# Optimization experiments

Measured on AMD Instinct MI355X. Metric: run time of the kernel, lower is better.

## Reference

```python
import jax, jax.numpy as jnp
import numpy as np

DIM = 512
N_HEADS = 8
HEAD_DIM = DIM // N_HEADS
BN_EPS = 1e-5


def setup_inputs() -> dict:
    key = jax.random.key(0)
    ks = jax.random.split(key, 8)
    B, C, H, W = 16, DIM, 32, 32
    x = jax.random.normal(ks[0], (B, C, H, W), dtype=jnp.float32)
    # 1x1 convs == channel matmuls: stacked q/k/v weights [3, out, in], proj [out, in]
    w_qkv = jax.random.normal(ks[1], (3, DIM, DIM), dtype=jnp.float32) * (DIM ** -0.5)
    w_proj = jax.random.normal(ks[2], (DIM, DIM), dtype=jnp.float32) * (DIM ** -0.5)
    # BatchNorm (inference form) params for q/k/v branches, stacked [3, C]
    bn_gamma = jax.random.uniform(ks[3], (3, DIM), minval=0.5, maxval=1.5)
    bn_beta = jax.random.normal(ks[4], (3, DIM)) * 0.1
    bn_mean = jax.random.normal(ks[5], (3, DIM)) * 0.1
    bn_var = jax.random.uniform(ks[6], (3, DIM), minval=0.5, maxval=1.5)
    return {"x": x, "w_qkv": w_qkv, "w_proj": w_proj, "bn_gamma": bn_gamma,
            "bn_beta": bn_beta, "bn_mean": bn_mean, "bn_var": bn_var}


def _ternary_ste(t):
    # forward: sign(t) in {-1,0,1}; backward: identity (straight-through)
    return t + jax.lax.stop_gradient(jnp.sign(t) - t)


def reference(x, w_qkv, w_proj, bn_gamma, bn_beta, bn_mean, bn_var):
    B, C, H, W = x.shape
    N = H * W
    xf = x.reshape(B, C, N)
    # fused 1x1 conv for q,k,v: [3,B,C,N]
    qkv = jnp.einsum('koc,bcn->kbon', w_qkv, xf)
    # BatchNorm (inference): y = (x - mean)/sqrt(var+eps)*gamma + beta
    s = bn_gamma / jnp.sqrt(bn_var + BN_EPS)          # [3,C]
    b = bn_beta - bn_mean * s                          # [3,C]
    qkv = qkv * s[:, None, :, None] + b[:, None, :, None]
    q = _ternary_ste(qkv[0]).reshape(B, N_HEADS, HEAD_DIM, N)
    k = _ternary_ste(qkv[1]).reshape(B, N_HEADS, HEAD_DIM, N)
    v = qkv[2].reshape(B, N_HEADS, HEAD_DIM, N)
    scale = HEAD_DIM ** -0.5
    attn = jnp.einsum('bhdn,bhen->bhde', q, k) * scale  # [B,h,d,d] channel-wise attn
    attn = jax.nn.softmax(attn, axis=-1)
    out = jnp.einsum('bhde,bhen->bhdn', attn, v).reshape(B, C, N)
    out = jnp.einsum('oc,bcn->bon', w_proj, out) + xf   # proj + residual
    return out.reshape(B, C, H, W)
```

## Files before the change

### kernel.cpp

```cpp
#include <hip/hip_runtime.h>
#include <math.h>

#define BN_EPS 1e-5f
#define FIXC 1.0e-4f

typedef _Float16 f16;
typedef _Float16 f16x4 __attribute__((ext_vector_type(4)));
typedef _Float16 f16x8 __attribute__((ext_vector_type(8)));
typedef float f32x4 __attribute__((ext_vector_type(4)));
typedef int i32x4 __attribute__((ext_vector_type(4)));

static constexpr int BB = 16;
static constexpr int C  = 512;
static constexpr int NP = 1024;
static constexpr int NH = 8;
static constexpr int HD = 64;
static constexpr int M3 = 1536;

static constexpr size_t OFF_WHI  = 0;
static constexpr size_t OFF_WLO  = 1572864;
static constexpr size_t OFF_WPH  = 3145728;
static constexpr size_t OFF_SB   = 3670016;
static constexpr size_t OFF_WN   = 3682304;
static constexpr size_t OFF_XN   = 3686400;
static constexpr size_t OFF_FLAG = 3751936;
static constexpr size_t OFF_XTH  = 5849088;
static constexpr size_t OFF_XTL  = 22626304;
static constexpr size_t OFF_AOT  = OFF_XTH;
static constexpr size_t OFF_Q    = 39403520;
static constexpr size_t OFF_K    = 47792128;
static constexpr size_t OFF_VT   = 56180736;

__device__ __forceinline__ void gld16(const void* g, void* l) {
  __builtin_amdgcn_global_load_lds(
      (const __attribute__((address_space(1))) void*)g,
      (__attribute__((address_space(3))) void*)l, 16, 0, 0);
}

__global__ __launch_bounds__(256) void k_convW(
    const float* __restrict__ wqkv, const float* __restrict__ wproj,
    const float* __restrict__ g, const float* __restrict__ be,
    const float* __restrict__ mu, const float* __restrict__ va,
    f16* __restrict__ Whi, f16* __restrict__ Wlo, f16* __restrict__ Wph,
    float* __restrict__ sA, float* __restrict__ bA)
{
  const int i = blockIdx.x * 256 + threadIdx.x;
  if (i < M3 * C) {
    const float w = wqkv[i];
    const f16 h = (f16)w;
    Whi[i] = h;
    Wlo[i] = (f16)(w - (float)h);
  }
  if (i < C * C) Wph[i] = (f16)wproj[i];
  if (i < M3) {
    const float s = g[i] / sqrtf(va[i] + BN_EPS);
    sA[i] = s;
    bA[i] = be[i] - mu[i] * s;
  }
}

__global__ __launch_bounds__(256) void k_wnorm(
    const float* __restrict__ wqkv, float* __restrict__ wnorm)
{
  const int row = blockIdx.x * 4 + (threadIdx.x >> 6);
  const int lane = threadIdx.x & 63;
  const float4 v0 = *(const float4*)&wqkv[(size_t)row * C + lane * 8];
  const float4 v1 = *(const float4*)&wqkv[(size_t)row * C + lane * 8 + 4];
  float s = v0.x * v0.x + v0.y * v0.y + v0.z * v0.z + v0.w * v0.w
          + v1.x * v1.x + v1.y * v1.y + v1.z * v1.z + v1.w * v1.w;
  s += __shfl_xor(s, 1);  s += __shfl_xor(s, 2);  s += __shfl_xor(s, 4);
  s += __shfl_xor(s, 8);  s += __shfl_xor(s, 16); s += __shfl_xor(s, 32);
  if (lane == 0) wnorm[row] = sqrtf(s);
}

__global__ __launch_bounds__(256) void k_convX(
    const float* __restrict__ x, f16* __restrict__ XtH, f16* __restrict__ XtL,
    float* __restrict__ xnorm2)
{
  const int k0 = blockIdx.x * 64, n0 = blockIdx.y * 64, b = blockIdx.z;
  __shared__ float ls[64][65];
  const int t = threadIdx.x;
  const float* xp = x + ((size_t)b * C + k0) * NP + n0;
  const int c4 = (t & 15) * 4, r0 = t >> 4;
#pragma unroll
  for (int q = 0; q < 4; ++q) {
    const float4 v = *(const float4*)(xp + (size_t)(r0 + q * 16) * NP + c4);
    ls[r0 + q * 16][c4 + 0] = v.x; ls[r0 + q * 16][c4 + 1] = v.y;
    ls[r0 + q * 16][c4 + 2] = v.z; ls[r0 + q * 16][c4 + 3] = v.w;
  }
  __syncthreads();
  if (t < 64) {
    float s2 = 0.f;
#pragma unroll
    for (int q = 0; q < 64; ++q) { const float v = ls[q][t]; s2 = fmaf(v, v, s2); }
    atomicAdd(&xnorm2[(b << 10) + n0 + t], s2);
  }
  const int n = t >> 2, kk = (t & 3) * 16;
  f16x8 hv0 = {}, hv1 = {}, lv0 = {}, lv1 = {};
#pragma unroll
  for (int q = 0; q < 8; ++q) {
    float v = ls[kk + q][n];
    f16 h = (f16)v;
    hv0[q] = h; lv0[q] = (f16)(v - (float)h);
  }
#pragma unroll
  for (int q = 0; q < 8; ++q) {
    float v = ls[kk + 8 + q][n];
    f16 h = (f16)v;
    hv1[q] = h; lv1[q] = (f16)(v - (float)h);
  }
  const size_t o = ((size_t)b * NP + n0 + n) * C + k0 + kk;
  *(f16x8*)&XtH[o] = hv0; *(f16x8*)&XtH[o + 8] = hv1;
  *(f16x8*)&XtL[o] = lv0; *(f16x8*)&XtL[o + 8] = lv1;
}

__global__ __launch_bounds__(256) void k_qkv_mfma(
    const f16* __restrict__ Whi, const f16* __restrict__ XtH,
    const float* __restrict__ sA, const float* __restrict__ bA,
    const float* __restrict__ wnorm, const float* __restrict__ xnorm2,
    signed char* __restrict__ qw, signed char* __restrict__ kw,
    f16* __restrict__ vt, unsigned* __restrict__ flagbits)
{
  __shared__ __align__(16) f16 SMEM[16384];
  f16* Ah = SMEM;
  f16* Bh = SMEM + 8192;

  const int t = threadIdx.x, lane = t & 63, wid = t >> 6;
  const int n0 = blockIdx.x * 128, m0 = blockIdx.y * 128, b = blockIdx.z;

  const f16* A0h = Whi + (size_t)m0 * C;
  const f16* B0h = XtH + ((size_t)b * NP + n0) * C;

  f32x4 acc[4][4];
#pragma unroll
  for (int i = 0; i < 4; ++i)
#pragma unroll
    for (int j = 0; j < 4; ++j) acc[i][j] = (f32x4){0.f, 0.f, 0.f, 0.f};

  const int wm = wid >> 1, wn = wid & 1;
  const int lr = lane & 15, ls = lane >> 4;
  const int srow8 = wid * 8 + (lane >> 3);
  const int scol = (lane & 7) * 8;

  for (int kc = 0; kc < 512; kc += 64) {
#pragma unroll
    for (int r = 0; r < 4; ++r) {
      const size_t go = (size_t)(r * 32 + srow8) * C + kc + scol;
      const int lo = (r * 32 + wid * 8) * 64;
      gld16(A0h + go, &Ah[lo]);
      gld16(B0h + go, &Bh[lo]);
    }
    __syncthreads();
#pragma unroll
    for (int ksub = 0; ksub < 2; ++ksub) {
      f16x8 ah[4], bh[4];
#pragma unroll
      for (int i = 0; i < 4; ++i) {
        ah[i] = *(const f16x8*)&Ah[(wm * 64 + i * 16 + lr) * 64 + ksub * 32 + ls * 8];
        bh[i] = *(const f16x8*)&Bh[(wn * 64 + i * 16 + lr) * 64 + ksub * 32 + ls * 8];
      }
#pragma unroll
      for (int i = 0; i < 4; ++i)
#pragma unroll
        for (int j = 0; j < 4; ++j)
          acc[i][j] = __builtin_amdgcn_mfma_f32_16x16x32_f16(ah[i], bh[j], acc[i][j], 0, 0, 0);
    }
    __syncthreads();
  }

  const int kidx = m0 >> 9;
  if (kidx != 2) {
    signed char* dst0 = (kidx == 0) ? qw : kw;
    float xnrm[4];
#pragma unroll
    for (int j = 0; j < 4; ++j)
      xnrm[j] = sqrtf(xnorm2[(b << 10) + n0 + wn * 64 + j * 16 + lr]);
#pragma unroll
    for (int i = 0; i < 4; ++i) {
      float sv[4], bv[4], dl[4];
#pragma unroll
      for (int r = 0; r < 4; ++r) {
        const int o = m0 + wm * 64 + i * 16 + ls * 4 + r;
        sv[r] = sA[o]; bv[r] = bA[o];
        dl[r] = FIXC * wnorm[o] * sv[r];
      }
      const int oc0 = (m0 & 511) + wm * 64 + i * 16 + ls * 4;
      const int og0 = m0 + wm * 64 + i * 16 + ls * 4;
#pragma unroll
      for (int j = 0; j < 4; ++j) {
        const int n = n0 + wn * 64 + j * 16 + lr;
#pragma unroll
        for (int r = 0; r < 4; ++r) {
          const float z = fmaf(acc[i][j][r], sv[r], bv[r]);
          dst0[((size_t)b * C + oc0 + r) * NP + n] =
              (signed char)((z > 0.f) - (z < 0.f));
          if (fabsf(z) <= dl[r] * xnrm[j]) {
            const int of = og0 + r;
            atomicOr(&flagbits[(((size_t)b * NP + n) << 5) + (of >> 5)],
                     1u << (of & 31));
          }
        }
      }
    }
  } else {
    const int c0 = m0 & 511;
    for (int hf = 0; hf < 2; ++hf) {
      __syncthreads();
      if (wn == hf) {
#pragma unroll
        for (int i = 0; i < 4; ++i) {
          float sv[4], bv[4];
#pragma unroll
          for (int r = 0; r < 4; ++r) {
            const int o = m0 + wm * 64 + i * 16 + ls * 4 + r;
            sv[r] = sA[o]; bv[r] = bA[o];
          }
#pragma unroll
          for (int j = 0; j < 4; ++j) {
            f16x4 pk;
#pragma unroll
            for (int r = 0; r < 4; ++r)
              pk[r] = (f16)fmaf(acc[i][j][r], sv[r], bv[r]);
            *(f16x4*)&SMEM[(size_t)(j * 16 + lr) * 136 + wm * 64 + i * 16 + ls * 4] = pk;
          }
        }
      }
      __syncthreads();
      const int nl = t >> 2, cc = (t & 3) * 32;
      const f16* src = &SMEM[(size_t)nl * 136 + cc];
      f16x8 r0 = *(const f16x8*)(src + 0);
      f16x8 r1 = *(const f16x8*)(src + 8);
      f16x8 r2 = *(const f16x8*)(src + 16);
      f16x8 r3 = *(const f16x8*)(src + 24);
      f16* dstv = vt + ((size_t)b * NP + n0 + hf * 64 + nl) * C + c0 + cc;
      *(f16x8*)(dstv + 0)  = r0;
      *(f16x8*)(dstv + 8)  = r1;
      *(f16x8*)(dstv + 16) = r2;
      *(f16x8*)(dstv + 24) = r3;
    }
  }
}

__global__ __launch_bounds__(256) void k_fix(
    const unsigned* __restrict__ flagbits,
    const f16* __restrict__ Whi, const f16* __restrict__ Wlo,
    const f16* __restrict__ XtH, const f16* __restrict__ XtL,
    const float* __restrict__ sA, const float* __restrict__ bA,
    signed char* __restrict__ qw, signed char* __restrict__ kw)
{
  const int wv = blockIdx.x * 4 + (threadIdx.x >> 6);
  const int lane = threadIdx.x & 63;
  const int b = wv >> 10, n = wv & 1023;

  const unsigned* bm = flagbits + ((size_t)wv << 5);
  const unsigned myw = (lane < 32) ? bm[lane] : 0u;
  if (__ballot(myw != 0) == 0ULL) return;

  const size_t xo = ((size_t)b * NP + n) * C + lane * 8;
  const f16x8 bhv = *(const f16x8*)&XtH[xo];
  const f16x8 blv = *(const f16x8*)&XtL[xo];
  float xv[8];
#pragma unroll
  for (int q = 0; q < 8; ++q) xv[q] = (float)bhv[q] + (float)blv[q];

  for (int w = 0; w < 32; ++w) {
    unsigned bits = __shfl(myw, w);
    while (bits) {
      const int o = w * 32 + __builtin_ctz(bits);
      bits &= bits - 1;
      const f16x8 ahv = *(const f16x8*)&Whi[(size_t)o * C + lane * 8];
      const f16x8 alv = *(const f16x8*)&Wlo[(size_t)o * C + lane * 8];
      float s = 0.f;
#pragma unroll
      for (int q = 0; q < 8; ++q)
        s = fmaf((float)ahv[q] + (float)alv[q], xv[q], s);
      s += __shfl_xor(s, 1);  s += __shfl_xor(s, 2);  s += __shfl_xor(s, 4);
      s += __shfl_xor(s, 8);  s += __shfl_xor(s, 16); s += __shfl_xor(s, 32);
      if (lane == 0) {
        const float y = fmaf(s, sA[o], bA[o]);
        const signed char sg = (signed char)((y > 0.f) - (y < 0.f));
        if (o < 512) qw[((size_t)b * C + o) * NP + n] = sg;
        else         kw[((size_t)b * C + (o - 512)) * NP + n] = sg;
      }
    }
  }
}

__global__ __launch_bounds__(256) void k_attn_fused(
    const signed char* __restrict__ qw, const signed char* __restrict__ kw,
    const f16* __restrict__ vt, f16* __restrict__ aot)
{
  const int half = blockIdx.x;
  const int bh = blockIdx.y;
  const int b = bh >> 3, h = bh & 7;
  const int t = threadIdx.x, lane = t & 63, wid = t >> 6;
  const int dw = wid * 16;
  const int lr = lane & 15, lg = lane >> 4;

  __shared__ f16 ph[64][72];
  __shared__ f16 pl[64][72];
  __shared__ f16 sb[64][72];

  const signed char* qp = qw + ((size_t)b * C + h * HD + dw + lr) * NP;
  const signed char* kp = kw + ((size_t)b * C + h * HD + lr) * NP;

  i32x4 accS[4];
#pragma unroll
  for (int j = 0; j < 4; ++j) accS[j] = (i32x4){0, 0, 0, 0};

#pragma unroll 4
  for (int ks = 0; ks < 16; ++ks) {
    const i32x4 af = *(const i32x4*)(qp + ks * 64 + lg * 16);
#pragma unroll
    for (int j = 0; j < 4; ++j) {
      const i32x4 bf = *(const i32x4*)(kp + (size_t)(j * 16) * NP + ks * 64 + lg * 16);
      accS[j] = __builtin_amdgcn_mfma_i32_16x16x64_i8(af, bf, accS[j], 0, 0, 0);
    }
  }

#pragma unroll
  for (int r = 0; r < 4; ++r) {
    float mx = (float)accS[0][r];
#pragma unroll
    for (int j = 1; j < 4; ++j) mx = fmaxf(mx, (float)accS[j][r]);
    mx = fmaxf(mx, __shfl_xor(mx, 1));
    mx = fmaxf(mx, __shfl_xor(mx, 2));
    mx = fmaxf(mx, __shfl_xor(mx, 4));
    mx = fmaxf(mx, __shfl_xor(mx, 8));
    float pvv[4];
    float sm = 0.f;
#pragma unroll
    for (int j = 0; j < 4; ++j) {
      pvv[j] = expf(((float)accS[j][r] - mx) * 0.125f);
      sm += pvv[j];
    }
    sm += __shfl_xor(sm, 1);
    sm += __shfl_xor(sm, 2);
    sm += __shfl_xor(sm, 4);
    sm += __shfl_xor(sm, 8);
    const float inv = 1.f / sm;
    const int drow = dw + lg * 4 + r;
#pragma unroll
    for (int j = 0; j < 4; ++j) {
      const float p = pvv[j] * inv;
      const f16 hi = (f16)p;
      ph[drow][j * 16 + lr] = hi;
      pl[drow][j * 16 + lr] = (f16)(p - (float)hi);
    }
  }
  __syncthreads();

  const f16x8 pa0h = *(const f16x8*)&ph[dw + lr][lg * 8];
  const f16x8 pa0l = *(const f16x8*)&pl[dw + lr][lg * 8];
  const f16x8 pa1h = *(const f16x8*)&ph[dw + lr][32 + lg * 8];
  const f16x8 pa1l = *(const f16x8*)&pl[dw + lr][32 + lg * 8];

  const f16* vbase = vt + (size_t)b * NP * C + h * HD;
  const int nbase = half * 512;

  for (int nc = 0; nc < 8; ++nc) {
    const int nn0 = nbase + nc * 64;
    __syncthreads();
#pragma unroll
    for (int nt = 0; nt < 4; ++nt) {
      const f16* vp = vbase + (size_t)(nn0 + nt * 16 + lr) * C + lg * 8;
      const f16x8 bv0 = *(const f16x8*)(vp);
      const f16x8 bv1 = *(const f16x8*)(vp + 32);
      f32x4 acc = (f32x4){0.f, 0.f, 0.f, 0.f};
      acc = __builtin_amdgcn_mfma_f32_16x16x32_f16(pa0h, bv0, acc, 0, 0, 0);
      acc = __builtin_amdgcn_mfma_f32_16x16x32_f16(pa0l, bv0, acc, 0, 0, 0);
      acc = __builtin_amdgcn_mfma_f32_16x16x32_f16(pa1h, bv1, acc, 0, 0, 0);
      acc = __builtin_amdgcn_mfma_f32_16x16x32_f16(pa1l, bv1, acc, 0, 0, 0);
      f16x4 pk;
#pragma unroll
      for (int r = 0; r < 4; ++r) pk[r] = (f16)acc[r];
      *(f16x4*)&sb[nt * 16 + lr][dw + lg * 4] = pk;
    }
    __syncthreads();
    const int nl = t >> 2, cc = (t & 3) * 16;
    const f16x8 o0 = *(const f16x8*)&sb[nl][cc];
    const f16x8 o1 = *(const f16x8*)&sb[nl][cc + 8];
    f16* dst = aot + ((size_t)b * NP + nn0 + nl) * C + h * HD + cc;
    *(f16x8*)(dst + 0) = o0;
    *(f16x8*)(dst + 8) = o1;
  }
}

__global__ __launch_bounds__(256) void k_proj_mfma(
    const f16* __restrict__ Wph, const f16* __restrict__ aot,
    const float* __restrict__ X, float* __restrict__ out)
{
  __shared__ __align__(16) f16 Ah[128 * 32];
  __shared__ __align__(16) f16 Bh[128 * 32];

  const int t = threadIdx.x, lane = t & 63, wid = t >> 6;
  const int n0 = blockIdx.x * 128, m0 = blockIdx.y * 128, b = blockIdx.z;

  const f16* A0 = Wph + (size_t)m0 * C;
  const f16* B0 = aot + ((size_t)b * NP + n0) * C;

  f32x4 acc[4][4];
#pragma unroll
  for (int i = 0; i < 4; ++i)
#pragma unroll
    for (int j = 0; j < 4; ++j) acc[i][j] = (f32x4){0.f, 0.f, 0.f, 0.f};

  const int wm = wid >> 1, wn = wid & 1;
  const int lr = lane & 15, ls = lane >> 4;
  const int srow = wid * 16 + (lane >> 2);
  const int scol = (lane & 3) * 8;

  for (int kc = 0; kc < 512; kc += 32) {
#pragma unroll
    for (int r = 0; r < 2; ++r) {
      const size_t go = (size_t)(r * 64 + srow) * C + kc + scol;
      const int lo = (r * 64 + wid * 16) * 32;
      gld16(A0 + go, &Ah[lo]);
      gld16(B0 + go, &Bh[lo]);
    }
    __syncthreads();

    f16x8 ah[4], bh[4];
#pragma unroll
    for (int i = 0; i < 4; ++i) {
      ah[i] = *(const f16x8*)&Ah[(wm * 64 + i * 16 + lr) * 32 + ls * 8];
      bh[i] = *(const f16x8*)&Bh[(wn * 64 + i * 16 + lr) * 32 + ls * 8];
    }
#pragma unroll
    for (int i = 0; i < 4; ++i)
#pragma unroll
      for (int j = 0; j < 4; ++j)
        acc[i][j] = __builtin_amdgcn_mfma_f32_16x16x32_f16(ah[i], bh[j], acc[i][j], 0, 0, 0);
    __syncthreads();
  }

#pragma unroll
  for (int i = 0; i < 4; ++i) {
    const int oc0 = m0 + wm * 64 + i * 16 + ls * 4;
#pragma unroll
    for (int j = 0; j < 4; ++j) {
      const int n = n0 + wn * 64 + j * 16 + lr;
#pragma unroll
      for (int r = 0; r < 4; ++r) {
        const size_t idx = ((size_t)b * C + oc0 + r) * NP + n;
        out[idx] = acc[i][j][r] + X[idx];
      }
    }
  }
}

extern "C" void kernel_launch(void* const* d_in, const int* in_sizes, int n_in,
                              void* d_out, int out_size, void* d_ws, size_t ws_size,
                              hipStream_t stream)
{
  const float* x      = (const float*)d_in[0];
  const float* w_qkv  = (const float*)d_in[1];
  const float* w_proj = (const float*)d_in[2];
  const float* g      = (const float*)d_in[3];
  const float* be     = (const float*)d_in[4];
  const float* mu     = (const float*)d_in[5];
  const float* va     = (const float*)d_in[6];
  float* out = (float*)d_out;

  char* ws = (char*)d_ws;
  f16*  Whi = (f16*)(ws + OFF_WHI);
  f16*  Wlo = (f16*)(ws + OFF_WLO);
  f16*  Wph = (f16*)(ws + OFF_WPH);
  float* sA = (float*)(ws + OFF_SB);
  float* bA = sA + M3;
  float* wn = (float*)(ws + OFF_WN);
  float* xn2 = (float*)(ws + OFF_XN);
  unsigned* flagbits = (unsigned*)(ws + OFF_FLAG);
  f16*  XtH = (f16*)(ws + OFF_XTH);
  f16*  XtL = (f16*)(ws + OFF_XTL);
  f16*  aot = (f16*)(ws + OFF_AOT);
  signed char* qw = (signed char*)(ws + OFF_Q);
  signed char* kw = (signed char*)(ws + OFF_K);
  f16*  vtw = (f16*)(ws + OFF_VT);

  hipMemsetAsync(xn2, 0, OFF_XTH - OFF_XN, stream);

  k_convW<<<dim3((M3 * C + 255) / 256), 256, 0, stream>>>(
      w_qkv, w_proj, g, be, mu, va, Whi, Wlo, Wph, sA, bA);
  k_wnorm<<<dim3(256), 256, 0, stream>>>(w_qkv, wn);
  k_convX<<<dim3(C / 64, NP / 64, BB), 256, 0, stream>>>(x, XtH, XtL, xn2);
  k_qkv_mfma<<<dim3(NP / 128, M3 / 128, BB), 256, 0, stream>>>(
      Whi, XtH, sA, bA, wn, xn2, qw, kw, vtw, flagbits);
  k_fix<<<dim3(BB * NP / 4), 256, 0, stream>>>(
      flagbits, Whi, Wlo, XtH, XtL, sA, bA, qw, kw);
  k_attn_fused<<<dim3(2, BB * NH), 256, 0, stream>>>(qw, kw, vtw, aot);
  k_proj_mfma<<<dim3(NP / 128, C / 128, BB), 256, 0, stream>>>(Wph, aot, x, out);
}
```

Before: 144.1 us.

## Store fp16 GEMM operands in MFMA fragment-tiled layout for contiguous LDS reads

The high-precision fp16 halves of W_qkv, X^T, W_proj and the attention output are now written in a tile/k-block fragment order. Each wave's global-to-LDS copies and its MFMA operand reads then become contiguous per-lane 16-byte accesses rather than strided row reads, which are meant to avoid LDS bank conflicts and simplify addressing. The projection GEMM also moves to a 64-wide K step per barrier. Weight conversion is vectorized to 8 elements per thread with fewer blocks. In exchange, the producer kernels (convX, attention epilogue, fix) do more scattered global writes and reads through the fragment index function.

```diff
diff --git a/kernel.cpp b/kernel.cpp
--- a/kernel.cpp
+++ b/kernel.cpp
@@ -16,6 +16,7 @@
 static constexpr int NH = 8;
 static constexpr int HD = 64;
 static constexpr int M3 = 1536;
+
 
 static constexpr size_t OFF_WHI  = 0;
 static constexpr size_t OFF_WLO  = 1572864;
@@ -37,6 +38,11 @@
       (__attribute__((address_space(3))) void*)l, 16, 0, 0);
 }
 
+__device__ __forceinline__ size_t frag_off(int tile, int kt, int row7, int k5) {
+  return (((size_t)tile * 16 + kt) * 8 + (row7 >> 4)) * 512
+       + (size_t)((row7 & 15) | ((k5 >> 3) << 4)) * 8;
+}
+
 __global__ __launch_bounds__(256) void k_convW(
     const float* __restrict__ wqkv, const float* __restrict__ wproj,
     const float* __restrict__ g, const float* __restrict__ be,
@@ -45,13 +51,30 @@
     float* __restrict__ sA, float* __restrict__ bA)
 {
   const int i = blockIdx.x * 256 + threadIdx.x;
-  if (i < M3 * C) {
-    const float w = wqkv[i];
-    const f16 h = (f16)w;
-    Whi[i] = h;
-    Wlo[i] = (f16)(w - (float)h);
-  }
-  if (i < C * C) Wph[i] = (f16)wproj[i];
+  {
+    const int m = i >> 6, l = i & 63;
+    const float4 v0 = *(const float4*)&wqkv[(size_t)m * C + l * 8];
+    const float4 v1 = *(const float4*)&wqkv[(size_t)m * C + l * 8 + 4];
+    const float vv[8] = {v0.x, v0.y, v0.z, v0.w, v1.x, v1.y, v1.z, v1.w};
+    f16x8 hv, lv;
+#pragma unroll
+    for (int q = 0; q < 8; ++q) {
+      const f16 h = (f16)vv[q];
+      hv[q] = h; lv[q] = (f16)(vv[q] - (float)h);
+    }
+    *(f16x8*)&Whi[frag_off(m >> 7, l >> 2, m & 127, (l & 3) * 8)] = hv;
+    *(f16x8*)&Wlo[(size_t)m * C + l * 8] = lv;
+  }
+  if (i < 32768) {
+    const int m = i >> 6, l = i & 63;
+    const float4 v0 = *(const float4*)&wproj[(size_t)m * C + l * 8];
+    const float4 v1 = *(const float4*)&wproj[(size_t)m * C + l * 8 + 4];
+    const float vv[8] = {v0.x, v0.y, v0.z, v0.w, v1.x, v1.y, v1.z, v1.w};
+    f16x8 hv;
+#pragma unroll
+    for (int q = 0; q < 8; ++q) hv[q] = (f16)vv[q];
+    *(f16x8*)&Wph[frag_off(m >> 7, l >> 2, m & 127, (l & 3) * 8)] = hv;
+  }
   if (i < M3) {
     const float s = g[i] / sqrtf(va[i] + BN_EPS);
     sA[i] = s;
@@ -96,22 +119,25 @@
     atomicAdd(&xnorm2[(b << 10) + n0 + t], s2);
   }
   const int n = t >> 2, kk = (t & 3) * 16;
+  const int n_abs = n0 + n;
   f16x8 hv0 = {}, hv1 = {}, lv0 = {}, lv1 = {};
 #pragma unroll
   for (int q = 0; q < 8; ++q) {
-    float v = ls[kk + q][n];
-    f16 h = (f16)v;
+    const float v = ls[kk + q][n];
+    const f16 h = (f16)v;
     hv0[q] = h; lv0[q] = (f16)(v - (float)h);
   }
 #pragma unroll
   for (int q = 0; q < 8; ++q) {
-    float v = ls[kk + 8 + q][n];
-    f16 h = (f16)v;
+    const float v = ls[kk + 8 + q][n];
+    const f16 h = (f16)v;
     hv1[q] = h; lv1[q] = (f16)(v - (float)h);
   }
-  const size_t o = ((size_t)b * NP + n0 + n) * C + k0 + kk;
-  *(f16x8*)&XtH[o] = hv0; *(f16x8*)&XtH[o + 8] = hv1;
-  *(f16x8*)&XtL[o] = lv0; *(f16x8*)&XtL[o + 8] = lv1;
+  const int kb0 = k0 + kk, kb1 = k0 + kk + 8;
+  *(f16x8*)&XtH[frag_off(b * 8 + (n_abs >> 7), kb0 >> 5, n_abs & 127, kb0 & 31)] = hv0;
+  *(f16x8*)&XtH[frag_off(b * 8 + (n_abs >> 7), kb1 >> 5, n_abs & 127, kb1 & 31)] = hv1;
+  *(f16x8*)&XtL[((size_t)b * NP + n_abs) * C + kb0] = lv0;
+  *(f16x8*)&XtL[((size_t)b * NP + n_abs) * C + kb1] = lv1;
 }
 
 __global__ __launch_bounds__(256) void k_qkv_mfma(
@@ -122,14 +148,14 @@
     f16* __restrict__ vt, unsigned* __restrict__ flagbits)
 {
   __shared__ __align__(16) f16 SMEM[16384];
-  f16* Ah = SMEM;
-  f16* Bh = SMEM + 8192;
+  f16* As = SMEM;
+  f16* Bs = SMEM + 8192;
 
   const int t = threadIdx.x, lane = t & 63, wid = t >> 6;
   const int n0 = blockIdx.x * 128, m0 = blockIdx.y * 128, b = blockIdx.z;
 
-  const f16* A0h = Whi + (size_t)m0 * C;
-  const f16* B0h = XtH + ((size_t)b * NP + n0) * C;
+  const f16* Af = Whi + (size_t)(m0 >> 7) * 65536;
+  const f16* Bf = XtH + ((size_t)b * 8 + (n0 >> 7)) * 65536;
 
   f32x4 acc[4][4];
 #pragma unroll
@@ -139,16 +165,15 @@
 
   const int wm = wid >> 1, wn = wid & 1;
   const int lr = lane & 15, ls = lane >> 4;
-  const int srow8 = wid * 8 + (lane >> 3);
-  const int scol = (lane & 7) * 8;
-
-  for (int kc = 0; kc < 512; kc += 64) {
+  const int soff = wid * 512 + lane * 8;
+
+  for (int kt = 0; kt < 16; kt += 2) {
+    const f16* Ak = Af + (size_t)kt * 4096;
+    const f16* Bk = Bf + (size_t)kt * 4096;
 #pragma unroll
     for (int r = 0; r < 4; ++r) {
-      const size_t go = (size_t)(r * 32 + srow8) * C + kc + scol;
-      const int lo = (r * 32 + wid * 8) * 64;
-      gld16(A0h + go, &Ah[lo]);
-      gld16(B0h + go, &Bh[lo]);
+      gld16(Ak + r * 2048 + soff, &As[r * 2048 + wid * 512]);
+      gld16(Bk + r * 2048 + soff, &Bs[r * 2048 + wid * 512]);
     }
     __syncthreads();
 #pragma unroll
@@ -156,8 +181,8 @@
       f16x8 ah[4], bh[4];
 #pragma unroll
       for (int i = 0; i < 4; ++i) {
-        ah[i] = *(const f16x8*)&Ah[(wm * 64 + i * 16 + lr) * 64 + ksub * 32 + ls * 8];
-        bh[i] = *(const f16x8*)&Bh[(wn * 64 + i * 16 + lr) * 64 + ksub * 32 + ls * 8];
+        ah[i] = *(const f16x8*)&As[ksub * 4096 + (wm * 4 + i) * 512 + lane * 8];
+        bh[i] = *(const f16x8*)&Bs[ksub * 4096 + (wn * 4 + i) * 512 + lane * 8];
       }
 #pragma unroll
       for (int i = 0; i < 4; ++i)
@@ -256,9 +281,10 @@
   const unsigned myw = (lane < 32) ? bm[lane] : 0u;
   if (__ballot(myw != 0) == 0ULL) return;
 
-  const size_t xo = ((size_t)b * NP + n) * C + lane * 8;
-  const f16x8 bhv = *(const f16x8*)&XtH[xo];
-  const f16x8 blv = *(const f16x8*)&XtL[xo];
+  const int kb = lane * 8;
+  const f16x8 bhv = *(const f16x8*)&XtH[
+      frag_off(b * 8 + (n >> 7), kb >> 5, n & 127, kb & 31)];
+  const f16x8 blv = *(const f16x8*)&XtL[((size_t)b * NP + n) * C + kb];
   float xv[8];
 #pragma unroll
   for (int q = 0; q < 8; ++q) xv[q] = (float)bhv[q] + (float)blv[q];
@@ -268,8 +294,9 @@
     while (bits) {
       const int o = w * 32 + __builtin_ctz(bits);
       bits &= bits - 1;
-      const f16x8 ahv = *(const f16x8*)&Whi[(size_t)o * C + lane * 8];
-      const f16x8 alv = *(const f16x8*)&Wlo[(size_t)o * C + lane * 8];
+      const f16x8 ahv = *(const f16x8*)&Whi[
+          frag_off(o >> 7, kb >> 5, o & 127, kb & 31)];
+      const f16x8 alv = *(const f16x8*)&Wlo[(size_t)o * C + kb];
       float s = 0.f;
 #pragma unroll
       for (int q = 0; q < 8; ++q)
@@ -380,9 +407,11 @@
     const int nl = t >> 2, cc = (t & 3) * 16;
     const f16x8 o0 = *(const f16x8*)&sb[nl][cc];
     const f16x8 o1 = *(const f16x8*)&sb[nl][cc + 8];
-    f16* dst = aot + ((size_t)b * NP + nn0 + nl) * C + h * HD + cc;
-    *(f16x8*)(dst + 0) = o0;
-    *(f16x8*)(dst + 8) = o1;
+    const int n_abs = nn0 + nl;
+    const int c1 = h * HD + cc, c2 = h * HD + cc + 8;
+    aot += 0;
+    *(f16x8*)&aot[frag_off(b * 8 + (n_abs >> 7), c1 >> 5, n_abs & 127, c1 & 31)] = o0;
+    *(f16x8*)&aot[frag_off(b * 8 + (n_abs >> 7), c2 >> 5, n_abs & 127, c2 & 31)] = o1;
   }
 }
 
@@ -390,14 +419,15 @@
     const f16* __restrict__ Wph, const f16* __restrict__ aot,
     const float* __restrict__ X, float* __restrict__ out)
 {
-  __shared__ __align__(16) f16 Ah[128 * 32];
-  __shared__ __align__(16) f16 Bh[128 * 32];
+  __shared__ __align__(16) f16 SMEM[16384];
+  f16* As = SMEM;
+  f16* Bs = SMEM + 8192;
 
   const int t = threadIdx.x, lane = t & 63, wid = t >> 6;
   const int n0 = blockIdx.x * 128, m0 = blockIdx.y * 128, b = blockIdx.z;
 
-  const f16* A0 = Wph + (size_t)m0 * C;
-  const f16* B0 = aot + ((size_t)b * NP + n0) * C;
+  const f16* Af = Wph + (size_t)(m0 >> 7) * 65536;
+  const f16* Bf = aot + ((size_t)b * 8 + (n0 >> 7)) * 65536;
 
   f32x4 acc[4][4];
 #pragma unroll
@@ -407,30 +437,31 @@
 
   const int wm = wid >> 1, wn = wid & 1;
   const int lr = lane & 15, ls = lane >> 4;
-  const int srow = wid * 16 + (lane >> 2);
-  const int scol = (lane & 3) * 8;
-
-  for (int kc = 0; kc < 512; kc += 32) {
-#pragma unroll
-    for (int r = 0; r < 2; ++r) {
-      const size_t go = (size_t)(r * 64 + srow) * C + kc + scol;
-      const int lo = (r * 64 + wid * 16) * 32;
-      gld16(A0 + go, &Ah[lo]);
-      gld16(B0 + go, &Bh[lo]);
+  const int soff = wid * 512 + lane * 8;
+
+  for (int kt = 0; kt < 16; kt += 2) {
+    const f16* Ak = Af + (size_t)kt * 4096;
+    const f16* Bk = Bf + (size_t)kt * 4096;
+#pragma unroll
+    for (int r = 0; r < 4; ++r) {
+      gld16(Ak + r * 2048 + soff, &As[r * 2048 + wid * 512]);
+      gld16(Bk + r * 2048 + soff, &Bs[r * 2048 + wid * 512]);
     }
     __syncthreads();
-
-    f16x8 ah[4], bh[4];
-#pragma unroll
-    for (int i = 0; i < 4; ++i) {
-      ah[i] = *(const f16x8*)&Ah[(wm * 64 + i * 16 + lr) * 32 + ls * 8];
-      bh[i] = *(const f16x8*)&Bh[(wn * 64 + i * 16 + lr) * 32 + ls * 8];
-    }
-#pragma unroll
-    for (int i = 0; i < 4; ++i)
-#pragma unroll
-      for (int j = 0; j < 4; ++j)
-        acc[i][j] = __builtin_amdgcn_mfma_f32_16x16x32_f16(ah[i], bh[j], acc[i][j], 0, 0, 0);
+#pragma unroll
+    for (int ksub = 0; ksub < 2; ++ksub) {
+      f16x8 ah[4], bh[4];
+#pragma unroll
+      for (int i = 0; i < 4; ++i) {
+        ah[i] = *(const f16x8*)&As[ksub * 4096 + (wm * 4 + i) * 512 + lane * 8];
+        bh[i] = *(const f16x8*)&Bs[ksub * 4096 + (wn * 4 + i) * 512 + lane * 8];
+      }
+#pragma unroll
+      for (int i = 0; i < 4; ++i)
+#pragma unroll
+        for (int j = 0; j < 4; ++j)
+          acc[i][j] = __builtin_amdgcn_mfma_f32_16x16x32_f16(ah[i], bh[j], acc[i][j], 0, 0, 0);
+    }
     __syncthreads();
   }
 
@@ -480,7 +511,7 @@
 
   hipMemsetAsync(xn2, 0, OFF_XTH - OFF_XN, stream);
 
-  k_convW<<<dim3((M3 * C + 255) / 256), 256, 0, stream>>>(
+  k_convW<<<dim3(384), 256, 0, stream>>>(
       w_qkv, w_proj, g, be, mu, va, Whi, Wlo, Wph, sA, bA);
   k_wnorm<<<dim3(256), 256, 0, stream>>>(w_qkv, wn);
   k_convX<<<dim3(C / 64, NP / 64, BB), 256, 0, stream>>>(x, XtH, XtL, xn2);
```

New measurement: 142.0 us. Within noise of the previous version (-1.5%).
